# Performance work log

Measured on AMD Instinct MI355X. Metric: run time of the kernel, lower is better.

The kernel has to match this reference:

```python
import jax, jax.numpy as jnp
import numpy as np

HEADS = 8
CH = 64  # channel_head
SCALE = CH ** -0.5


def rmsnorm2d(x, g):
    # F.normalize(x, dim=1) * g * sqrt(C)  (lucidrains conv RMSNorm)
    c = x.shape[1]
    n = jnp.sqrt(jnp.sum(x * x, axis=1, keepdims=True))
    return x / jnp.maximum(n, 1e-12) * g[None, :, None, None] * (c ** 0.5)


def setup_inputs() -> dict:
    key = jax.random.key(0)
    ks = jax.random.split(key, 3)
    B, C, H, W = 8, 512, 64, 64
    hidden = HEADS * CH  # 512
    x = jax.random.normal(ks[0], (B, C, H, W), dtype=jnp.float32)
    norm_g = jnp.ones((C,), dtype=jnp.float32)
    qkv_w = jax.random.normal(ks[1], (3 * hidden, C), dtype=jnp.float32) * 0.02
    ffn_w = jax.random.normal(ks[2], (C, hidden), dtype=jnp.float32) * 0.02
    ffn_b = jnp.zeros((C,), dtype=jnp.float32)
    ffn_norm_g = jnp.ones((C,), dtype=jnp.float32)
    return {"x": x, "norm_g": norm_g, "qkv_w": qkv_w, "ffn_w": ffn_w,
            "ffn_b": ffn_b, "ffn_norm_g": ffn_norm_g}


def reference(x, norm_g, qkv_w, ffn_w, ffn_b, ffn_norm_g):
    b, c, h, w = x.shape
    n = h * w
    residual = x
    xn = rmsnorm2d(x, norm_g)
    # 1x1 conv == channel matmul: [b, 3*hidden, h, w]
    qkv = jnp.einsum('bchw,oc->bohw', xn, qkv_w)
    q, k, v = jnp.split(qkv, 3, axis=1)

    def to_heads(t):
        # b (h c) x y -> b h (x y) c
        t = t.reshape(b, HEADS, CH, n)
        return jnp.transpose(t, (0, 1, 3, 2))  # [b, heads, n, ch]

    q, k, v = to_heads(q), to_heads(k), to_heads(v)
    q = jax.nn.softmax(q, axis=-1) * SCALE   # softmax over channel dim
    k = jax.nn.softmax(k, axis=-2)           # softmax over sequence dim
    attn = jnp.einsum('bhnc,bhnd->bhcd', k, v)    # [b, heads, ch, ch]
    out = jnp.einsum('bhnc,bhcd->bhnd', q, attn)  # [b, heads, n, ch]
    # b h (x y) c -> b (h c) x y
    out = jnp.transpose(out, (0, 1, 3, 2)).reshape(b, HEADS * CH, h, w)
    # ffn: 1x1 conv (with bias) + RMSNorm
    out = jnp.einsum('bchw,oc->bohw', out, ffn_w) + ffn_b[None, :, None, None]
    out = rmsnorm2d(out, ffn_norm_g)
    return out + residual
```

## Files before the change

### kernel.cpp

```cpp
#include <hip/hip_runtime.h>


typedef __bf16 bf16_t;
typedef __bf16 bf8 __attribute__((ext_vector_type(8)));
typedef float f32x4 __attribute__((ext_vector_type(4)));

#define NC 512
#define NP 4096
#define SQRTC 22.62741699796952f
#define QSCALE 0.125f
#define QSTRIDE  ((size_t)NC * NP)
#define KVSTRIDE ((size_t)1024 * NP)
#define LDC 136

__device__ inline unsigned short bfbits(__bf16 h) {
    return __builtin_bit_cast(unsigned short, h);
}

__device__ __forceinline__ void gload_lds16(const bf16_t* g, __bf16* l) {
    __builtin_amdgcn_global_load_lds(
        (const __attribute__((address_space(1))) void*)g,
        (__attribute__((address_space(3))) void*)l, 16, 0, 0);
}

__global__ __launch_bounds__(256) void
wconv_kernel(const float* __restrict__ qkv_w, const float* __restrict__ g,
             const float* __restrict__ ffn_w, bf16_t* __restrict__ Wg,
             bf16_t* __restrict__ Wf) {
    const int bx = blockIdx.x;
    if (bx < 768) {
        int i0 = (bx * 256 + threadIdx.x) * 4;
        float4 wv = *(const float4*)&qkv_w[i0];
        const float4 gv = *(const float4*)&g[i0 & 511];
        ushort4 o;
        o.x = bfbits((__bf16)(wv.x * gv.x));
        o.y = bfbits((__bf16)(wv.y * gv.y));
        o.z = bfbits((__bf16)(wv.z * gv.z));
        o.w = bfbits((__bf16)(wv.w * gv.w));
        *(ushort4*)&Wg[i0] = o;
    } else {
        int i0 = ((bx - 768) * 256 + threadIdx.x) * 4;
        float4 wv = *(const float4*)&ffn_w[i0];
        ushort4 o;
        o.x = bfbits((__bf16)wv.x);
        o.y = bfbits((__bf16)wv.y);
        o.z = bfbits((__bf16)wv.z);
        o.w = bfbits((__bf16)wv.w);
        *(ushort4*)&Wf[i0] = o;
    }
}

__global__ __launch_bounds__(512) void
norm_transpose_kernel(const float* __restrict__ x, bf16_t* __restrict__ xnT) {
    const int bl = blockIdx.y;
    const int p0 = blockIdx.x * 32;
    const int t = threadIdx.x;
    const float* xb = x + (size_t)bl * QSTRIDE;
    bf16_t* ob = xnT + (size_t)bl * QSTRIDE;

    const int cg = t & 7, r0 = t >> 3;
    f32x4 ss = {0.f, 0.f, 0.f, 0.f};
    #pragma unroll
    for (int k = 0; k < 8; ++k) {
        const int c = r0 + k * 64;
        float4 v = *(const float4*)&xb[(size_t)c * NP + p0 + cg * 4];
        ss.x += v.x * v.x; ss.y += v.y * v.y;
        ss.z += v.z * v.z; ss.w += v.w * v.w;
    }
    #pragma unroll
    for (int m = 8; m <= 32; m <<= 1) {
        ss.x += __shfl_xor(ss.x, m); ss.y += __shfl_xor(ss.y, m);
        ss.z += __shfl_xor(ss.z, m); ss.w += __shfl_xor(ss.w, m);
    }
    __shared__ float sP[8][34];
    __shared__ float sInv[32];
    const int w = t >> 6;
    if ((t & 63) < 8) {
        const int p = (t & 7) * 4;
        sP[w][p] = ss.x; sP[w][p + 1] = ss.y;
        sP[w][p + 2] = ss.z; sP[w][p + 3] = ss.w;
    }
    __syncthreads();
    if (t < 32) {
        float tot = 0.f;
        #pragma unroll
        for (int j = 0; j < 8; ++j) tot += sP[j][t];
        sInv[t] = SQRTC / fmaxf(sqrtf(tot), 1e-12f);
    }
    __syncthreads();

    __shared__ __bf16 sT[128][41];
    for (int cc = 0; cc < 512; cc += 128) {
        #pragma unroll
        for (int j = 0; j < 2; ++j) {
            int idx = t + j * 512;
            int cr = idx >> 3, pg = idx & 7;
            float4 v = *(const float4*)&xb[(size_t)(cc + cr) * NP + p0 + pg * 4];
            sT[cr][pg * 4 + 0] = (__bf16)(v.x * sInv[pg * 4 + 0]);
            sT[cr][pg * 4 + 1] = (__bf16)(v.y * sInv[pg * 4 + 1]);
            sT[cr][pg * 4 + 2] = (__bf16)(v.z * sInv[pg * 4 + 2]);
            sT[cr][pg * 4 + 3] = (__bf16)(v.w * sInv[pg * 4 + 3]);
        }
        __syncthreads();
        {
            int p = t >> 4, c8 = (t & 15) * 8;
            bf8 v;
            #pragma unroll
            for (int q = 0; q < 8; ++q) v[q] = sT[c8 + q][p];
            *(bf8*)&ob[(size_t)(p0 + p) * NC + cc + c8] = v;
        }
        __syncthreads();
    }
}

__global__ __launch_bounds__(256) void
gemm_qkv_kernel(const bf16_t* __restrict__ Wg, const bf16_t* __restrict__ xnT,
                bf16_t* __restrict__ qout, bf16_t* __restrict__ kvout) {
    const int bn = blockIdx.x, bm = blockIdx.y, b = blockIdx.z;
    const int t = threadIdx.x;
    const int w = t >> 6, ln = t & 63, quad = ln >> 4, l16 = ln & 15;
    const int wm = w >> 1, wn = w & 1;

    __shared__ __align__(16) __bf16 sAB[128 * LDC];
    __bf16* const sA = sAB;
    __bf16* const sB = sAB + 8192;

    f32x4 acc[4][4] = {};
    const bf16_t* Abase = Wg + (size_t)(bm * 128) * NC;
    const bf16_t* Bbase = xnT + (size_t)b * QSTRIDE + (size_t)(bn * 128) * NC;

    const int lrow = ln >> 3;
    const int lkc = ((ln & 7) ^ lrow) * 8;
    const int xr = l16 & 7;

    for (int kt = 0; kt < 8; ++kt) {
        const int k0 = kt * 64;
        #pragma unroll
        for (int i = 0; i < 4; ++i) {
            const int chunk = w * 4 + i;
            const int row = chunk * 8 + lrow;
            gload_lds16(Abase + (size_t)row * NC + k0 + lkc, &sA[chunk * 512]);
            gload_lds16(Bbase + (size_t)row * NC + k0 + lkc, &sB[chunk * 512]);
        }
        __syncthreads();
        #pragma unroll
        for (int ks = 0; ks < 2; ++ks) {
            bf8 af[4], bfr[4];
            const int kx = ((ks * 4 + quad) ^ xr) << 3;
            #pragma unroll
            for (int mi = 0; mi < 4; ++mi)
                af[mi] = *(const bf8*)&sA[(wm * 64 + mi * 16 + l16) * 64 + kx];
            #pragma unroll
            for (int ni = 0; ni < 4; ++ni)
                bfr[ni] = *(const bf8*)&sB[(wn * 64 + ni * 16 + l16) * 64 + kx];
            #pragma unroll
            for (int mi = 0; mi < 4; ++mi)
                #pragma unroll
                for (int ni = 0; ni < 4; ++ni)
                    acc[mi][ni] = __builtin_amdgcn_mfma_f32_16x16x32_bf16(
                        af[mi], bfr[ni], acc[mi][ni], 0, 0, 0);
        }
        __syncthreads();
    }

    {
        const int rbase = wm * 64 + quad * 4;
        const int cbase = wn * 64 + l16;
        #pragma unroll
        for (int mi = 0; mi < 4; ++mi)
            #pragma unroll
            for (int ni = 0; ni < 4; ++ni)
                #pragma unroll
                for (int r = 0; r < 4; ++r)
                    sAB[(rbase + mi * 16 + r) * LDC + cbase + ni * 16] =
                        (__bf16)acc[mi][ni][r];
    }
    __syncthreads();
    bf16_t* qb = qout + (size_t)b * QSTRIDE;
    bf16_t* kvb = kvout + (size_t)b * KVSTRIDE;
    const int p0 = bn * 128;
    #pragma unroll
    for (int i = 0; i < 8; ++i) {
        int e = t + i * 256;
        int rr = e >> 4, seg = (e & 15) * 8;
        bf8 v = *(const bf8*)&sAB[rr * LDC + seg];
        int row = bm * 128 + rr;
        if (row < 512)
            *(bf8*)&qb[(size_t)row * NP + p0 + seg] = v;
        else
            *(bf8*)&kvb[(size_t)(row - 512) * NP + p0 + seg] = v;
    }
}

__global__ __launch_bounds__(256) void
gemm_ffn_kernel(const bf16_t* __restrict__ Wf, const bf16_t* __restrict__ xoT,
                const float* __restrict__ bias, bf16_t* __restrict__ y,
                float* __restrict__ ysq) {
    const int bn = blockIdx.x, bm = blockIdx.y, b = blockIdx.z;
    const int t = threadIdx.x;
    const int w = t >> 6, ln = t & 63, quad = ln >> 4, l16 = ln & 15;
    const int wm = w >> 1, wn = w & 1;

    __shared__ __align__(16) __bf16 sAB[128 * LDC];
    __bf16* const sA = sAB;
    __bf16* const sB = sAB + 8192;

    f32x4 acc[4][4] = {};
    const bf16_t* Abase = Wf + (size_t)(bm * 128) * NC;
    const bf16_t* Bbase = xoT + (size_t)b * KVSTRIDE + (size_t)(bn * 128) * NC;

    const int lrow = ln >> 3;
    const int lkc = ((ln & 7) ^ lrow) * 8;
    const int xr = l16 & 7;

    for (int kt = 0; kt < 8; ++kt) {
        const int k0 = kt * 64;
        #pragma unroll
        for (int i = 0; i < 4; ++i) {
            const int chunk = w * 4 + i;
            const int row = chunk * 8 + lrow;
            gload_lds16(Abase + (size_t)row * NC + k0 + lkc, &sA[chunk * 512]);
            gload_lds16(Bbase + (size_t)row * NC + k0 + lkc, &sB[chunk * 512]);
        }
        __syncthreads();
        #pragma unroll
        for (int ks = 0; ks < 2; ++ks) {
            bf8 af[4], bfr[4];
            const int kx = ((ks * 4 + quad) ^ xr) << 3;
            #pragma unroll
            for (int mi = 0; mi < 4; ++mi)
                af[mi] = *(const bf8*)&sA[(wm * 64 + mi * 16 + l16) * 64 + kx];
            #pragma unroll
            for (int ni = 0; ni < 4; ++ni)
                bfr[ni] = *(const bf8*)&sB[(wn * 64 + ni * 16 + l16) * 64 + kx];
            #pragma unroll
            for (int mi = 0; mi < 4; ++mi)
                #pragma unroll
                for (int ni = 0; ni < 4; ++ni)
                    acc[mi][ni] = __builtin_amdgcn_mfma_f32_16x16x32_bf16(
                        af[mi], bfr[ni], acc[mi][ni], 0, 0, 0);
        }
        __syncthreads();
    }

    float* sq = ysq + (size_t)b * NP;
    const int p0 = bn * 128;
    {
        const int rbase = wm * 64 + quad * 4;
        #pragma unroll
        for (int ni = 0; ni < 4; ++ni) {
            const int col = p0 + wn * 64 + ni * 16 + l16;
            float colsq = 0.f;
            #pragma unroll
            for (int mi = 0; mi < 4; ++mi) {
                #pragma unroll
                for (int r = 0; r < 4; ++r) {
                    const int row = bm * 128 + rbase + mi * 16 + r;
                    __bf16 vb = (__bf16)(acc[mi][ni][r] + bias[row]);
                    sAB[(rbase + mi * 16 + r) * LDC + wn * 64 + ni * 16 + l16] = vb;
                    float vf = (float)vb;
                    colsq += vf * vf;
                }
            }
            colsq += __shfl_xor(colsq, 16);
            colsq += __shfl_xor(colsq, 32);
            if (quad == 0) atomicAdd(&sq[col], colsq);
        }
    }
    __syncthreads();
    bf16_t* yb = y + (size_t)b * QSTRIDE;
    #pragma unroll
    for (int i = 0; i < 8; ++i) {
        int e = t + i * 256;
        int rr = e >> 4, seg = (e & 15) * 8;
        bf8 v = *(const bf8*)&sAB[rr * LDC + seg];
        *(bf8*)&yb[(size_t)(bm * 128 + rr) * NP + p0 + seg] = v;
    }
}

__global__ __launch_bounds__(256) void
kstats_kernel(const bf16_t* __restrict__ kv, float* __restrict__ kmax,
              float* __restrict__ kinv) {
    const int oc = blockIdx.x, b = blockIdx.y;
    const int t = threadIdx.x, w = t >> 6, ln = t & 63;

    const bf16_t* row = kv + (size_t)b * KVSTRIDE + (size_t)oc * NP;
    float v[16];
    bf8 x0 = *(const bf8*)&row[t * 8];
    bf8 x1 = *(const bf8*)&row[2048 + t * 8];
    #pragma unroll
    for (int j = 0; j < 8; ++j) { v[j] = (float)x0[j]; v[8 + j] = (float)x1[j]; }

    float m = v[0];
    #pragma unroll
    for (int j = 1; j < 16; ++j) m = fmaxf(m, v[j]);
    #pragma unroll
    for (int off = 32; off > 0; off >>= 1) m = fmaxf(m, __shfl_down(m, off));
    __shared__ float sR[4];
    __shared__ float sS[4];
    if (ln == 0) sR[w] = m;
    __syncthreads();
    m = fmaxf(fmaxf(sR[0], sR[1]), fmaxf(sR[2], sR[3]));

    float s = 0.f;
    #pragma unroll
    for (int j = 0; j < 16; ++j) s += __expf(v[j] - m);
    #pragma unroll
    for (int off = 32; off > 0; off >>= 1) s += __shfl_down(s, off);
    if (ln == 0) sS[w] = s;
    __syncthreads();
    if (t == 0) {
        kmax[b * 512 + oc] = m;
        kinv[b * 512 + oc] = 1.0f / (sS[0] + sS[1] + sS[2] + sS[3]);
    }
}

__global__ __launch_bounds__(256) void
attn_kernel(const bf16_t* __restrict__ kv, const float* __restrict__ kmax,
            float* __restrict__ attnP) {
    const int h = blockIdx.x, ks = blockIdx.y, b = blockIdx.z;
    const int t = threadIdx.x, w = t >> 6, ln = t & 63, quad = ln >> 4, l16 = ln & 15;

    const bf16_t* Kb = kv + (size_t)b * KVSTRIDE + (size_t)(h * 64) * NP;
    const bf16_t* Vb = kv + (size_t)b * KVSTRIDE + (size_t)(512 + h * 64 + w * 16) * NP;

    float km[4];
    #pragma unroll
    for (int mi = 0; mi < 4; ++mi) km[mi] = kmax[b * 512 + h * 64 + mi * 16 + l16];

    f32x4 acc[4] = {};
    const int pbase = ks * 512 + quad * 8;
    #pragma unroll 4
    for (int it = 0; it < 16; ++it) {
        const int p0 = pbase + it * 32;
        bf8 bfr = *(const bf8*)&Vb[(size_t)l16 * NP + p0];
        #pragma unroll
        for (int mi = 0; mi < 4; ++mi) {
            bf8 kr = *(const bf8*)&Kb[(size_t)(mi * 16 + l16) * NP + p0];
            bf8 af;
            #pragma unroll
            for (int j = 0; j < 8; ++j)
                af[j] = (__bf16)__expf((float)kr[j] - km[mi]);
            acc[mi] = __builtin_amdgcn_mfma_f32_16x16x32_bf16(af, bfr, acc[mi], 0, 0, 0);
        }
    }

    float* outp = attnP + (((size_t)(b * 8 + h) * 8 + ks) << 12);
    #pragma unroll
    for (int mi = 0; mi < 4; ++mi) {
        float4 v;
        v.x = acc[mi][0]; v.y = acc[mi][1]; v.z = acc[mi][2]; v.w = acc[mi][3];
        *(float4*)&outp[(w * 16 + l16) * 64 + mi * 16 + quad * 4] = v;
    }
}

__global__ __launch_bounds__(256) void
attnsum_kernel(const float* __restrict__ attnP, const float* __restrict__ kinv,
               bf16_t* __restrict__ attnF, float* __restrict__ ysq) {
    const int gtid = (blockIdx.x * 4 + blockIdx.y) * 256 + threadIdx.x;
    if (gtid < 8 * NP) ysq[gtid] = 0.f;

    const int bh = blockIdx.x;
    const int e0 = blockIdx.y * 1024 + threadIdx.x * 4;
    const float* ap = attnP + ((size_t)bh << 15);
    float4 s = {0.f, 0.f, 0.f, 0.f};
    #pragma unroll
    for (int ks = 0; ks < 8; ++ks) {
        float4 v = *(const float4*)&ap[(ks << 12) + e0];
        s.x += v.x; s.y += v.y; s.z += v.z; s.w += v.w;
    }
    const float* kvp = kinv + (bh >> 3) * 512 + (bh & 7) * 64;
    const int c = e0 & 63;
    ushort4 o;
    o.x = bfbits((__bf16)(s.x * kvp[c]));
    o.y = bfbits((__bf16)(s.y * kvp[c + 1]));
    o.z = bfbits((__bf16)(s.z * kvp[c + 2]));
    o.w = bfbits((__bf16)(s.w * kvp[c + 3]));
    *(ushort4*)&attnF[((size_t)bh << 12) + e0] = o;
}

__global__ __launch_bounds__(256) void
outgemm_kernel(const bf16_t* __restrict__ q, const bf16_t* __restrict__ attnF,
               bf16_t* __restrict__ xoT) {
    const int pt = blockIdx.x, h = blockIdx.y, b = blockIdx.z;
    const int p0 = pt * 128;
    const int t = threadIdx.x, w = t >> 6, ln = t & 63, quad = ln >> 4, l16 = ln & 15;

    __shared__ __align__(16) __bf16 sQb[128][72];

    const bf16_t* aF = attnF + ((size_t)(b * 8 + h) << 12);
    bf8 bfr[2][4];
    #pragma unroll
    for (int ksp = 0; ksp < 2; ++ksp)
        #pragma unroll
        for (int ni = 0; ni < 4; ++ni)
            bfr[ksp][ni] = *(const bf8*)&aF[(ni * 16 + l16) * 64 + ksp * 32 + quad * 8];

    const bf16_t* qb = q + (size_t)b * QSTRIDE;
    #pragma unroll
    for (int i = 0; i < 32; ++i) {
        int e = t + i * 256;
        int c = e >> 7, p = e & 127;
        sQb[p][c] = qb[(size_t)(h * 64 + c) * NP + p0 + p];
    }
    __syncthreads();

    #pragma unroll
    for (int pass = 0; pass < 4; ++pass) {
        const int tok = pass * 32 + (t >> 3);
        const int c8 = (t & 7) * 8;
        bf8 v = *(const bf8*)&sQb[tok][c8];
        float f[8];
        #pragma unroll
        for (int j = 0; j < 8; ++j) f[j] = (float)v[j];
        float m = f[0];
        #pragma unroll
        for (int j = 1; j < 8; ++j) m = fmaxf(m, f[j]);
        #pragma unroll
        for (int off = 1; off < 8; off <<= 1) m = fmaxf(m, __shfl_xor(m, off));
        float s = 0.f;
        #pragma unroll
        for (int j = 0; j < 8; ++j) { f[j] = __expf(f[j] - m); s += f[j]; }
        #pragma unroll
        for (int off = 1; off < 8; off <<= 1) s += __shfl_xor(s, off);
        const float inv = QSCALE / s;
        #pragma unroll
        for (int j = 0; j < 8; ++j) v[j] = (__bf16)(f[j] * inv);
        *(bf8*)&sQb[tok][c8] = v;
    }
    __syncthreads();

    f32x4 acc[2][4] = {};
    #pragma unroll
    for (int ksp = 0; ksp < 2; ++ksp) {
        const int kk = ksp * 32;
        bf8 af[2];
        #pragma unroll
        for (int mi = 0; mi < 2; ++mi)
            af[mi] = *(const bf8*)&sQb[w * 32 + mi * 16 + l16][kk + quad * 8];
        #pragma unroll
        for (int mi = 0; mi < 2; ++mi)
            #pragma unroll
            for (int ni = 0; ni < 4; ++ni)
                acc[mi][ni] = __builtin_amdgcn_mfma_f32_16x16x32_bf16(
                    af[mi], bfr[ksp][ni], acc[mi][ni], 0, 0, 0);
    }
    __syncthreads();

    #pragma unroll
    for (int mi = 0; mi < 2; ++mi)
        #pragma unroll
        for (int ni = 0; ni < 4; ++ni)
            #pragma unroll
            for (int r = 0; r < 4; ++r)
                sQb[w * 32 + mi * 16 + quad * 4 + r][ni * 16 + l16] =
                    (__bf16)acc[mi][ni][r];
    __syncthreads();
    bf16_t* xob = xoT + (size_t)b * KVSTRIDE;
    #pragma unroll
    for (int i = 0; i < 4; ++i) {
        int e = t + i * 256;
        int rr = e >> 3, seg = (e & 7) * 8;
        bf8 v = *(const bf8*)&sQb[rr][seg];
        *(bf8*)&xob[(size_t)(p0 + rr) * NC + h * 64 + seg] = v;
    }
}

__global__ __launch_bounds__(256) void
final_kernel(const bf16_t* __restrict__ y, const float* __restrict__ ysq,
             const float* __restrict__ g2, const float* __restrict__ x,
             float* __restrict__ out) {
    const int b = blockIdx.y;
    int idx = blockIdx.x * 256 + threadIdx.x;
    int o = idx >> 9;
    int p8 = (idx & 511) * 8;
    const bf16_t* yb = y + (size_t)b * QSTRIDE;
    const float* xb = x + (size_t)b * QSTRIDE;
    float* outb = out + (size_t)b * QSTRIDE;
    const float* sq = ysq + (size_t)b * NP;

    bf8 yv = *(const bf8*)&yb[(size_t)o * NP + p8];
    float gv = g2[o] * SQRTC;
    float4 a = *(const float4*)&xb[(size_t)o * NP + p8];
    float4 b2 = *(const float4*)&xb[(size_t)o * NP + p8 + 4];
    float inb[8];
    #pragma unroll
    for (int j = 0; j < 8; ++j)
        inb[j] = 1.0f / fmaxf(sqrtf(sq[p8 + j]), 1e-12f);

    float4 r0, r1;
    r0.x = (float)yv[0] * inb[0] * gv + a.x;
    r0.y = (float)yv[1] * inb[1] * gv + a.y;
    r0.z = (float)yv[2] * inb[2] * gv + a.z;
    r0.w = (float)yv[3] * inb[3] * gv + a.w;
    r1.x = (float)yv[4] * inb[4] * gv + b2.x;
    r1.y = (float)yv[5] * inb[5] * gv + b2.y;
    r1.z = (float)yv[6] * inb[6] * gv + b2.z;
    r1.w = (float)yv[7] * inb[7] * gv + b2.w;
    *(float4*)&outb[(size_t)o * NP + p8] = r0;
    *(float4*)&outb[(size_t)o * NP + p8 + 4] = r1;
}

extern "C" void kernel_launch(void* const* d_in, const int* in_sizes, int n_in,
                              void* d_out, int out_size, void* d_ws, size_t ws_size,
                              hipStream_t stream) {
    const float* x     = (const float*)d_in[0];
    const float* g     = (const float*)d_in[1];
    const float* qkv_w = (const float*)d_in[2];
    const float* ffn_w = (const float*)d_in[3];
    const float* ffn_b = (const float*)d_in[4];
    const float* ffn_g = (const float*)d_in[5];
    float* out = (float*)d_out;
    bf16_t* kv = (bf16_t*)d_out;

    const size_t FULL_BYTES =
        (8 * QSTRIDE + 8 * QSTRIDE + 786432 + 262144) * sizeof(bf16_t) +
        (8 * 512 + 8 * 512 + 8 * (size_t)NP) * sizeof(float);
    const bool full = ws_size >= FULL_BYTES;

    bf16_t* q    = (bf16_t*)d_ws;
    bf16_t* xnT  = q + 8 * QSTRIDE;
    bf16_t* Wg   = xnT + (full ? 8 : 2) * QSTRIDE;
    float*  attnP = (float*)xnT;
    bf16_t* attnF = Wg;
    bf16_t* Wf   = Wg + 786432;
    float*  kmax = (float*)(Wf + 262144);
    float*  kinv = kmax + 8 * 512;
    float*  ysq  = kinv + 8 * 512;

    wconv_kernel<<<dim3(1024), 256, 0, stream>>>(qkv_w, g, ffn_w, Wg, Wf);

    if (full) {
        norm_transpose_kernel<<<dim3(128, 8), 512, 0, stream>>>(x, xnT);
        gemm_qkv_kernel<<<dim3(32, 12, 8), 256, 0, stream>>>(Wg, xnT, q, kv);
    } else {
        for (int c = 0; c < 4; ++c) {
            norm_transpose_kernel<<<dim3(128, 2), 512, 0, stream>>>(
                x + (size_t)(2 * c) * QSTRIDE, xnT);
            gemm_qkv_kernel<<<dim3(32, 12, 2), 256, 0, stream>>>(
                Wg, xnT, q + (size_t)(2 * c) * QSTRIDE,
                kv + (size_t)(2 * c) * KVSTRIDE);
        }
    }

    kstats_kernel<<<dim3(512, 8), 256, 0, stream>>>(kv, kmax, kinv);
    attn_kernel<<<dim3(8, 8, 8), 256, 0, stream>>>(kv, kmax, attnP);
    attnsum_kernel<<<dim3(64, 4), 256, 0, stream>>>(attnP, kinv, attnF, ysq);
    outgemm_kernel<<<dim3(32, 8, 8), 256, 0, stream>>>(q, attnF, kv);
    gemm_ffn_kernel<<<dim3(32, 4, 8), 256, 0, stream>>>(Wf, kv, ffn_b, q, ysq);
    final_kernel<<<dim3(1024, 8), 256, 0, stream>>>(q, ysq, ffn_g, x, out);
}
```

Measured before the change: 305.1 us.

## Fold attention context into FFN weights and fuse q softmax into QKV GEMM

Instead of computing q·attn per head and then multiplying by the FFN weight, the FFN weight is premultiplied by each batch's per-head attention matrix in a small wmix kernel. The FFN GEMM then consumes softmaxed q directly, which removes the separate outgemm pass. The q softmax over channels moves into the QKV GEMM epilogue, which now writes q token-major. Weight conversion is folded into the norm/transpose kernel, and the FFN output is written as fp32 straight into the output buffer for the final residual pass, avoiding the bf16 intermediate. This removes a full activation-sized GEMM pass and several round trips, at the cost of per-batch weight matrices and fp32 intermediate traffic.

New measurement: 304.3 us. Within noise of the previous version (-0.3%).

```diff
diff --git a/kernel.cpp b/kernel.cpp
--- a/kernel.cpp
+++ b/kernel.cpp
@@ -51,10 +51,40 @@
 }
 
 __global__ __launch_bounds__(512) void
-norm_transpose_kernel(const float* __restrict__ x, bf16_t* __restrict__ xnT) {
+norm_transpose_kernel(const float* __restrict__ x, bf16_t* __restrict__ xnT,
+                      const float* __restrict__ qkv_w, const float* __restrict__ g,
+                      const float* __restrict__ ffn_w, bf16_t* __restrict__ Wg,
+                      bf16_t* __restrict__ Wf, int doW) {
     const int bl = blockIdx.y;
     const int p0 = blockIdx.x * 32;
     const int t = threadIdx.x;
+
+    if (doW) {
+        const int bid = blockIdx.y * 128 + blockIdx.x;
+        if (bid < 512) {
+            int i0 = bid * 2048 + t * 4;
+            if (i0 < 786432) {
+                float4 wv = *(const float4*)&qkv_w[i0];
+                const float4 gv = *(const float4*)&g[i0 & 511];
+                ushort4 o;
+                o.x = bfbits((__bf16)(wv.x * gv.x));
+                o.y = bfbits((__bf16)(wv.y * gv.y));
+                o.z = bfbits((__bf16)(wv.z * gv.z));
+                o.w = bfbits((__bf16)(wv.w * gv.w));
+                *(ushort4*)&Wg[i0] = o;
+            } else {
+                int j0 = i0 - 786432;
+                float4 wv = *(const float4*)&ffn_w[j0];
+                ushort4 o;
+                o.x = bfbits((__bf16)wv.x);
+                o.y = bfbits((__bf16)wv.y);
+                o.z = bfbits((__bf16)wv.z);
+                o.w = bfbits((__bf16)wv.w);
+                *(ushort4*)&Wf[j0] = o;
+            }
+        }
+    }
+
     const float* xb = x + (size_t)bl * QSTRIDE;
     bf16_t* ob = xnT + (size_t)bl * QSTRIDE;
 
@@ -163,118 +193,74 @@
         __syncthreads();
     }
 
-    {
-        const int rbase = wm * 64 + quad * 4;
-        const int cbase = wn * 64 + l16;
+    const int p0 = bn * 128;
+    if (bm < 4) {
         #pragma unroll
         for (int mi = 0; mi < 4; ++mi)
             #pragma unroll
             for (int ni = 0; ni < 4; ++ni)
                 #pragma unroll
                 for (int r = 0; r < 4; ++r)
-                    sAB[(rbase + mi * 16 + r) * LDC + cbase + ni * 16] =
-                        (__bf16)acc[mi][ni][r];
-    }
-    __syncthreads();
-    bf16_t* qb = qout + (size_t)b * QSTRIDE;
-    bf16_t* kvb = kvout + (size_t)b * KVSTRIDE;
-    const int p0 = bn * 128;
-    #pragma unroll
-    for (int i = 0; i < 8; ++i) {
-        int e = t + i * 256;
-        int rr = e >> 4, seg = (e & 15) * 8;
-        bf8 v = *(const bf8*)&sAB[rr * LDC + seg];
-        int row = bm * 128 + rr;
-        if (row < 512)
-            *(bf8*)&qb[(size_t)row * NP + p0 + seg] = v;
-        else
-            *(bf8*)&kvb[(size_t)(row - 512) * NP + p0 + seg] = v;
-    }
-}
-
-__global__ __launch_bounds__(256) void
-gemm_ffn_kernel(const bf16_t* __restrict__ Wf, const bf16_t* __restrict__ xoT,
-                const float* __restrict__ bias, bf16_t* __restrict__ y,
-                float* __restrict__ ysq) {
-    const int bn = blockIdx.x, bm = blockIdx.y, b = blockIdx.z;
-    const int t = threadIdx.x;
-    const int w = t >> 6, ln = t & 63, quad = ln >> 4, l16 = ln & 15;
-    const int wm = w >> 1, wn = w & 1;
-
-    __shared__ __align__(16) __bf16 sAB[128 * LDC];
-    __bf16* const sA = sAB;
-    __bf16* const sB = sAB + 8192;
-
-    f32x4 acc[4][4] = {};
-    const bf16_t* Abase = Wf + (size_t)(bm * 128) * NC;
-    const bf16_t* Bbase = xoT + (size_t)b * KVSTRIDE + (size_t)(bn * 128) * NC;
-
-    const int lrow = ln >> 3;
-    const int lkc = ((ln & 7) ^ lrow) * 8;
-    const int xr = l16 & 7;
-
-    for (int kt = 0; kt < 8; ++kt) {
-        const int k0 = kt * 64;
-        #pragma unroll
-        for (int i = 0; i < 4; ++i) {
-            const int chunk = w * 4 + i;
-            const int row = chunk * 8 + lrow;
-            gload_lds16(Abase + (size_t)row * NC + k0 + lkc, &sA[chunk * 512]);
-            gload_lds16(Bbase + (size_t)row * NC + k0 + lkc, &sB[chunk * 512]);
-        }
-        __syncthreads();
-        #pragma unroll
-        for (int ks = 0; ks < 2; ++ks) {
-            bf8 af[4], bfr[4];
-            const int kx = ((ks * 4 + quad) ^ xr) << 3;
+                    sAB[(wn * 64 + ni * 16 + l16) * LDC +
+                        wm * 64 + mi * 16 + quad * 4 + r] = (__bf16)acc[mi][ni][r];
+        __syncthreads();
+        {
+            __bf16* rp = &sAB[(t & 127) * LDC + (t >> 7) * 64];
+            float m = -1e30f;
+            #pragma unroll
+            for (int gg = 0; gg < 8; ++gg) {
+                bf8 v = *(const bf8*)&rp[gg * 8];
+                #pragma unroll
+                for (int j = 0; j < 8; ++j) m = fmaxf(m, (float)v[j]);
+            }
+            float s = 0.f;
+            #pragma unroll
+            for (int gg = 0; gg < 8; ++gg) {
+                bf8 v = *(const bf8*)&rp[gg * 8];
+                #pragma unroll
+                for (int j = 0; j < 8; ++j) s += __expf((float)v[j] - m);
+            }
+            const float inv = QSCALE / s;
+            #pragma unroll
+            for (int gg = 0; gg < 8; ++gg) {
+                bf8 v = *(const bf8*)&rp[gg * 8];
+                #pragma unroll
+                for (int j = 0; j < 8; ++j)
+                    v[j] = (__bf16)(__expf((float)v[j] - m) * inv);
+                *(bf8*)&rp[gg * 8] = v;
+            }
+        }
+        __syncthreads();
+        bf16_t* qb = qout + (size_t)b * QSTRIDE;
+        #pragma unroll
+        for (int i = 0; i < 8; ++i) {
+            int e = t + i * 256;
+            int p = e >> 4, c8 = (e & 15) * 8;
+            bf8 v = *(const bf8*)&sAB[p * LDC + c8];
+            *(bf8*)&qb[(size_t)(p0 + p) * NC + bm * 128 + c8] = v;
+        }
+    } else {
+        {
+            const int rbase = wm * 64 + quad * 4;
+            const int cbase = wn * 64 + l16;
             #pragma unroll
             for (int mi = 0; mi < 4; ++mi)
-                af[mi] = *(const bf8*)&sA[(wm * 64 + mi * 16 + l16) * 64 + kx];
-            #pragma unroll
-            for (int ni = 0; ni < 4; ++ni)
-                bfr[ni] = *(const bf8*)&sB[(wn * 64 + ni * 16 + l16) * 64 + kx];
-            #pragma unroll
-            for (int mi = 0; mi < 4; ++mi)
                 #pragma unroll
                 for (int ni = 0; ni < 4; ++ni)
-                    acc[mi][ni] = __builtin_amdgcn_mfma_f32_16x16x32_bf16(
-                        af[mi], bfr[ni], acc[mi][ni], 0, 0, 0);
-        }
-        __syncthreads();
-    }
-
-    float* sq = ysq + (size_t)b * NP;
-    const int p0 = bn * 128;
-    {
-        const int rbase = wm * 64 + quad * 4;
-        #pragma unroll
-        for (int ni = 0; ni < 4; ++ni) {
-            const int col = p0 + wn * 64 + ni * 16 + l16;
-            float colsq = 0.f;
-            #pragma unroll
-            for (int mi = 0; mi < 4; ++mi) {
-                #pragma unroll
-                for (int r = 0; r < 4; ++r) {
-                    const int row = bm * 128 + rbase + mi * 16 + r;
-                    __bf16 vb = (__bf16)(acc[mi][ni][r] + bias[row]);
-                    sAB[(rbase + mi * 16 + r) * LDC + wn * 64 + ni * 16 + l16] = vb;
-                    float vf = (float)vb;
-                    colsq += vf * vf;
-                }
-            }
-            colsq += __shfl_xor(colsq, 16);
-            colsq += __shfl_xor(colsq, 32);
-            if (quad == 0) atomicAdd(&sq[col], colsq);
-        }
-    }
-    __syncthreads();
-    bf16_t* yb = y + (size_t)b * QSTRIDE;
-    #pragma unroll
-    for (int i = 0; i < 8; ++i) {
-        int e = t + i * 256;
-        int rr = e >> 4, seg = (e & 15) * 8;
-        bf8 v = *(const bf8*)&sAB[rr * LDC + seg];
-        *(bf8*)&yb[(size_t)(bm * 128 + rr) * NP + p0 + seg] = v;
+                    #pragma unroll
+                    for (int r = 0; r < 4; ++r)
+                        sAB[(rbase + mi * 16 + r) * LDC + cbase + ni * 16] =
+                            (__bf16)acc[mi][ni][r];
+        }
+        __syncthreads();
+        bf16_t* kvb = kvout + (size_t)b * KVSTRIDE;
+        #pragma unroll
+        for (int i = 0; i < 8; ++i) {
+            int e = t + i * 256;
+            int rr = e >> 4, seg = (e & 15) * 8;
+            bf8 v = *(const bf8*)&sAB[rr * LDC + seg];
+            *(bf8*)&kvb[(size_t)(bm * 128 + rr - 512) * NP + p0 + seg] = v;
+        }
     }
 }
 
@@ -380,106 +366,165 @@
 }
 
 __global__ __launch_bounds__(256) void
-outgemm_kernel(const bf16_t* __restrict__ q, const bf16_t* __restrict__ attnF,
-               bf16_t* __restrict__ xoT) {
-    const int pt = blockIdx.x, h = blockIdx.y, b = blockIdx.z;
-    const int p0 = pt * 128;
+wmix_kernel(const bf16_t* __restrict__ Wf, const bf16_t* __restrict__ attnF,
+            bf16_t* __restrict__ Wff) {
+    const int om = blockIdx.x, h = blockIdx.y, b = blockIdx.z;
     const int t = threadIdx.x, w = t >> 6, ln = t & 63, quad = ln >> 4, l16 = ln & 15;
 
-    __shared__ __align__(16) __bf16 sQb[128][72];
-
+    __shared__ __bf16 sT[64][72];
     const bf16_t* aF = attnF + ((size_t)(b * 8 + h) << 12);
-    bf8 bfr[2][4];
-    #pragma unroll
-    for (int ksp = 0; ksp < 2; ++ksp)
+    #pragma unroll
+    for (int i = 0; i < 2; ++i) {
+        int e = t + i * 256;
+        int d = e >> 3, c8 = (e & 7) * 8;
+        bf8 v = *(const bf8*)&aF[d * 64 + c8];
+        #pragma unroll
+        for (int j = 0; j < 8; ++j) sT[c8 + j][d] = v[j];
+    }
+    __syncthreads();
+
+    const int obase = om * 128 + w * 32;
+    f32x4 acc[2][4] = {};
+    #pragma unroll
+    for (int kk = 0; kk < 2; ++kk) {
+        bf8 af[2], bfr[4];
+        #pragma unroll
+        for (int mi = 0; mi < 2; ++mi)
+            af[mi] = *(const bf8*)&Wf[(size_t)(obase + mi * 16 + l16) * NC +
+                                      h * 64 + kk * 32 + quad * 8];
         #pragma unroll
         for (int ni = 0; ni < 4; ++ni)
-            bfr[ksp][ni] = *(const bf8*)&aF[(ni * 16 + l16) * 64 + ksp * 32 + quad * 8];
-
-    const bf16_t* qb = q + (size_t)b * QSTRIDE;
-    #pragma unroll
-    for (int i = 0; i < 32; ++i) {
-        int e = t + i * 256;
-        int c = e >> 7, p = e & 127;
-        sQb[p][c] = qb[(size_t)(h * 64 + c) * NP + p0 + p];
-    }
-    __syncthreads();
-
-    #pragma unroll
-    for (int pass = 0; pass < 4; ++pass) {
-        const int tok = pass * 32 + (t >> 3);
-        const int c8 = (t & 7) * 8;
-        bf8 v = *(const bf8*)&sQb[tok][c8];
-        float f[8];
-        #pragma unroll
-        for (int j = 0; j < 8; ++j) f[j] = (float)v[j];
-        float m = f[0];
-        #pragma unroll
-        for (int j = 1; j < 8; ++j) m = fmaxf(m, f[j]);
-        #pragma unroll
-        for (int off = 1; off < 8; off <<= 1) m = fmaxf(m, __shfl_xor(m, off));
-        float s = 0.f;
-        #pragma unroll
-        for (int j = 0; j < 8; ++j) { f[j] = __expf(f[j] - m); s += f[j]; }
-        #pragma unroll
-        for (int off = 1; off < 8; off <<= 1) s += __shfl_xor(s, off);
-        const float inv = QSCALE / s;
-        #pragma unroll
-        for (int j = 0; j < 8; ++j) v[j] = (__bf16)(f[j] * inv);
-        *(bf8*)&sQb[tok][c8] = v;
-    }
-    __syncthreads();
-
-    f32x4 acc[2][4] = {};
-    #pragma unroll
-    for (int ksp = 0; ksp < 2; ++ksp) {
-        const int kk = ksp * 32;
-        bf8 af[2];
-        #pragma unroll
-        for (int mi = 0; mi < 2; ++mi)
-            af[mi] = *(const bf8*)&sQb[w * 32 + mi * 16 + l16][kk + quad * 8];
+            bfr[ni] = *(const bf8*)&sT[ni * 16 + l16][kk * 32 + quad * 8];
         #pragma unroll
         for (int mi = 0; mi < 2; ++mi)
             #pragma unroll
             for (int ni = 0; ni < 4; ++ni)
                 acc[mi][ni] = __builtin_amdgcn_mfma_f32_16x16x32_bf16(
-                    af[mi], bfr[ksp][ni], acc[mi][ni], 0, 0, 0);
-    }
-    __syncthreads();
-
+                    af[mi], bfr[ni], acc[mi][ni], 0, 0, 0);
+    }
+    bf16_t* outp = Wff + ((size_t)b << 18);
     #pragma unroll
     for (int mi = 0; mi < 2; ++mi)
         #pragma unroll
         for (int ni = 0; ni < 4; ++ni)
             #pragma unroll
-            for (int r = 0; r < 4; ++r)
-                sQb[w * 32 + mi * 16 + quad * 4 + r][ni * 16 + l16] =
-                    (__bf16)acc[mi][ni][r];
-    __syncthreads();
-    bf16_t* xob = xoT + (size_t)b * KVSTRIDE;
-    #pragma unroll
-    for (int i = 0; i < 4; ++i) {
-        int e = t + i * 256;
-        int rr = e >> 3, seg = (e & 7) * 8;
-        bf8 v = *(const bf8*)&sQb[rr][seg];
-        *(bf8*)&xob[(size_t)(p0 + rr) * NC + h * 64 + seg] = v;
-    }
-}
-
-__global__ __launch_bounds__(256) void
-final_kernel(const bf16_t* __restrict__ y, const float* __restrict__ ysq,
-             const float* __restrict__ g2, const float* __restrict__ x,
-             float* __restrict__ out) {
+            for (int r = 0; r < 4; ++r) {
+                int o = obase + mi * 16 + quad * 4 + r;
+                int c = ni * 16 + l16;
+                outp[(size_t)o * NC + h * 64 + c] = (__bf16)acc[mi][ni][r];
+            }
+}
+
+__global__ __launch_bounds__(256) void
+gemm_ffn_kernel(const bf16_t* __restrict__ Wff, const bf16_t* __restrict__ qsm,
+                const float* __restrict__ bias, float* __restrict__ out,
+                float* __restrict__ ysq) {
+    const int bn = blockIdx.x, bm = blockIdx.y, b = blockIdx.z;
+    const int t = threadIdx.x;
+    const int w = t >> 6, ln = t & 63, quad = ln >> 4, l16 = ln & 15;
+    const int wm = w >> 1, wn = w & 1;
+
+    __shared__ __align__(16) __bf16 sAB[128 * LDC];
+    __bf16* const sA = sAB;
+    __bf16* const sB = sAB + 8192;
+
+    f32x4 acc[4][4] = {};
+    const bf16_t* Abase = Wff + ((size_t)b << 18) + (size_t)(bm * 128) * NC;
+    const bf16_t* Bbase = qsm + (size_t)b * QSTRIDE + (size_t)(bn * 128) * NC;
+
+    const int lrow = ln >> 3;
+    const int lkc = ((ln & 7) ^ lrow) * 8;
+    const int xr = l16 & 7;
+
+    for (int kt = 0; kt < 8; ++kt) {
+        const int k0 = kt * 64;
+        #pragma unroll
+        for (int i = 0; i < 4; ++i) {
+            const int chunk = w * 4 + i;
+            const int row = chunk * 8 + lrow;
+            gload_lds16(Abase + (size_t)row * NC + k0 + lkc, &sA[chunk * 512]);
+            gload_lds16(Bbase + (size_t)row * NC + k0 + lkc, &sB[chunk * 512]);
+        }
+        __syncthreads();
+        #pragma unroll
+        for (int ks = 0; ks < 2; ++ks) {
+            bf8 af[4], bfr[4];
+            const int kx = ((ks * 4 + quad) ^ xr) << 3;
+            #pragma unroll
+            for (int mi = 0; mi < 4; ++mi)
+                af[mi] = *(const bf8*)&sA[(wm * 64 + mi * 16 + l16) * 64 + kx];
+            #pragma unroll
+            for (int ni = 0; ni < 4; ++ni)
+                bfr[ni] = *(const bf8*)&sB[(wn * 64 + ni * 16 + l16) * 64 + kx];
+            #pragma unroll
+            for (int mi = 0; mi < 4; ++mi)
+                #pragma unroll
+                for (int ni = 0; ni < 4; ++ni)
+                    acc[mi][ni] = __builtin_amdgcn_mfma_f32_16x16x32_bf16(
+                        af[mi], bfr[ni], acc[mi][ni], 0, 0, 0);
+        }
+        __syncthreads();
+    }
+
+    float* sq = ysq + (size_t)b * NP;
+    const int p0 = bn * 128;
+    const int rbase = wm * 64 + quad * 4;
+    #pragma unroll
+    for (int ni = 0; ni < 4; ++ni) {
+        const int col = p0 + wn * 64 + ni * 16 + l16;
+        float colsq = 0.f;
+        #pragma unroll
+        for (int mi = 0; mi < 4; ++mi)
+            #pragma unroll
+            for (int r = 0; r < 4; ++r) {
+                float vf = acc[mi][ni][r] + bias[bm * 128 + rbase + mi * 16 + r];
+                colsq += vf * vf;
+            }
+        colsq += __shfl_xor(colsq, 16);
+        colsq += __shfl_xor(colsq, 32);
+        if (quad == 0) atomicAdd(&sq[col], colsq);
+    }
+
+    float* sF = (float*)sAB;
+    float* ob = out + (size_t)b * QSTRIDE;
+    #pragma unroll
+    for (int half = 0; half < 2; ++half) {
+        __syncthreads();
+        if (wm == half) {
+            #pragma unroll
+            for (int mi = 0; mi < 4; ++mi)
+                #pragma unroll
+                for (int ni = 0; ni < 4; ++ni)
+                    #pragma unroll
+                    for (int r = 0; r < 4; ++r)
+                        sF[(quad * 4 + mi * 16 + r) * 136 + wn * 64 + ni * 16 + l16] =
+                            acc[mi][ni][r] +
+                            bias[bm * 128 + half * 64 + quad * 4 + mi * 16 + r];
+        }
+        __syncthreads();
+        #pragma unroll
+        for (int i = 0; i < 8; ++i) {
+            int e = t + i * 256;
+            int rr = e >> 5, c4 = (e & 31) * 4;
+            float4 v = *(const float4*)&sF[rr * 136 + c4];
+            *(float4*)&ob[(size_t)(bm * 128 + half * 64 + rr) * NP + p0 + c4] = v;
+        }
+    }
+}
+
+__global__ __launch_bounds__(256) void
+final_kernel(float* __restrict__ out, const float* __restrict__ ysq,
+             const float* __restrict__ g2, const float* __restrict__ x) {
     const int b = blockIdx.y;
     int idx = blockIdx.x * 256 + threadIdx.x;
     int o = idx >> 9;
     int p8 = (idx & 511) * 8;
-    const bf16_t* yb = y + (size_t)b * QSTRIDE;
+    float* ob = out + (size_t)b * QSTRIDE;
     const float* xb = x + (size_t)b * QSTRIDE;
-    float* outb = out + (size_t)b * QSTRIDE;
     const float* sq = ysq + (size_t)b * NP;
 
-    bf8 yv = *(const bf8*)&yb[(size_t)o * NP + p8];
+    float4 y0 = *(const float4*)&ob[(size_t)o * NP + p8];
+    float4 y1 = *(const float4*)&ob[(size_t)o * NP + p8 + 4];
     float gv = g2[o] * SQRTC;
     float4 a = *(const float4*)&xb[(size_t)o * NP + p8];
     float4 b2 = *(const float4*)&xb[(size_t)o * NP + p8 + 4];
@@ -489,16 +534,16 @@
         inb[j] = 1.0f / fmaxf(sqrtf(sq[p8 + j]), 1e-12f);
 
     float4 r0, r1;
-    r0.x = (float)yv[0] * inb[0] * gv + a.x;
-    r0.y = (float)yv[1] * inb[1] * gv + a.y;
-    r0.z = (float)yv[2] * inb[2] * gv + a.z;
-    r0.w = (float)yv[3] * inb[3] * gv + a.w;
-    r1.x = (float)yv[4] * inb[4] * gv + b2.x;
-    r1.y = (float)yv[5] * inb[5] * gv + b2.y;
-    r1.z = (float)yv[6] * inb[6] * gv + b2.z;
-    r1.w = (float)yv[7] * inb[7] * gv + b2.w;
-    *(float4*)&outb[(size_t)o * NP + p8] = r0;
-    *(float4*)&outb[(size_t)o * NP + p8 + 4] = r1;
+    r0.x = y0.x * inb[0] * gv + a.x;
+    r0.y = y0.y * inb[1] * gv + a.y;
+    r0.z = y0.z * inb[2] * gv + a.z;
+    r0.w = y0.w * inb[3] * gv + a.w;
+    r1.x = y1.x * inb[4] * gv + b2.x;
+    r1.y = y1.y * inb[5] * gv + b2.y;
+    r1.z = y1.z * inb[6] * gv + b2.z;
+    r1.w = y1.w * inb[7] * gv + b2.w;
+    *(float4*)&ob[(size_t)o * NP + p8] = r0;
+    *(float4*)&ob[(size_t)o * NP + p8 + 4] = r1;
 }
 
 extern "C" void kernel_launch(void* const* d_in, const int* in_sizes, int n_in,
@@ -523,20 +568,22 @@
     bf16_t* Wg   = xnT + (full ? 8 : 2) * QSTRIDE;
     float*  attnP = (float*)xnT;
     bf16_t* attnF = Wg;
+    bf16_t* Wff  = xnT;
     bf16_t* Wf   = Wg + 786432;
     float*  kmax = (float*)(Wf + 262144);
     float*  kinv = kmax + 8 * 512;
     float*  ysq  = kinv + 8 * 512;
 
-    wconv_kernel<<<dim3(1024), 256, 0, stream>>>(qkv_w, g, ffn_w, Wg, Wf);
-
     if (full) {
-        norm_transpose_kernel<<<dim3(128, 8), 512, 0, stream>>>(x, xnT);
+        norm_transpose_kernel<<<dim3(128, 8), 512, 0, stream>>>(
+            x, xnT, qkv_w, g, ffn_w, Wg, Wf, 1);
         gemm_qkv_kernel<<<dim3(32, 12, 8), 256, 0, stream>>>(Wg, xnT, q, kv);
     } else {
+        wconv_kernel<<<dim3(1024), 256, 0, stream>>>(qkv_w, g, ffn_w, Wg, Wf);
         for (int c = 0; c < 4; ++c) {
             norm_transpose_kernel<<<dim3(128, 2), 512, 0, stream>>>(
-                x + (size_t)(2 * c) * QSTRIDE, xnT);
+                x + (size_t)(2 * c) * QSTRIDE, xnT,
+                qkv_w, g, ffn_w, Wg, Wf, 0);
             gemm_qkv_kernel<<<dim3(32, 12, 2), 256, 0, stream>>>(
                 Wg, xnT, q + (size_t)(2 * c) * QSTRIDE,
                 kv + (size_t)(2 * c) * KVSTRIDE);
@@ -546,7 +593,7 @@
     kstats_kernel<<<dim3(512, 8), 256, 0, stream>>>(kv, kmax, kinv);
     attn_kernel<<<dim3(8, 8, 8), 256, 0, stream>>>(kv, kmax, attnP);
     attnsum_kernel<<<dim3(64, 4), 256, 0, stream>>>(attnP, kinv, attnF, ysq);
-    outgemm_kernel<<<dim3(32, 8, 8), 256, 0, stream>>>(q, attnF, kv);
-    gemm_ffn_kernel<<<dim3(32, 4, 8), 256, 0, stream>>>(Wf, kv, ffn_b, q, ysq);
-    final_kernel<<<dim3(1024, 8), 256, 0, stream>>>(q, ysq, ffn_g, x, out);
-}
+    wmix_kernel<<<dim3(4, 8, 8), 256, 0, stream>>>(Wf, attnF, Wff);
+    gemm_ffn_kernel<<<dim3(32, 4, 8), 256, 0, stream>>>(Wff, q, ffn_b, out, ysq);
+    final_kernel<<<dim3(1024, 8), 256, 0, stream>>>(out, ysq, ffn_g, x);
+}
```
